# Performance work log

Measured on AMD Instinct MI355X. Metric: run time of the kernel, lower is better.

The kernel has to match this reference:

```python
import jax, jax.numpy as jnp
import numpy as np

B, IN, CTRL, M, V, OUT = 2048, 64, 512, 1024, 64, 64


def setup_inputs() -> dict:
    key = jax.random.key(0)
    ks = jax.random.split(key, 20)
    s = 0.05  # small param scale for numerical stability

    def rn(k, shape, scale):
        return jax.random.normal(k, shape, dtype=jnp.float32) * scale

    return {
        # forward args
        "x": rn(ks[0], (B, IN), 1.0),
        "h_prev": rn(ks[1], (B, CTRL), 0.1),
        "c_prev": rn(ks[2], (B, CTRL), 0.1),
        "read_weights_prev": jax.nn.softmax(rn(ks[3], (B, M), 1.0), axis=1),
        # parameters
        "memory": rn(ks[4], (M, V), 1.0),
        "W_ih": rn(ks[5], (4 * CTRL, IN + V), s),
        "b_ih": rn(ks[6], (4 * CTRL,), s),
        "W_hh": rn(ks[7], (4 * CTRL, CTRL), s),
        "b_hh": rn(ks[8], (4 * CTRL,), s),
        "W_read": rn(ks[9], (M, CTRL), s),
        "b_read": rn(ks[10], (M,), s),
        "W_write": rn(ks[11], (M, CTRL), s),
        "b_write": rn(ks[12], (M,), s),
        "W_erase": rn(ks[13], (V, CTRL), s),
        "b_erase": rn(ks[14], (V,), s),
        "W_add": rn(ks[15], (V, CTRL), s),
        "b_add": rn(ks[16], (V,), s),
        "W_out": rn(ks[17], (OUT, CTRL + V), s),
        "b_out": rn(ks[18], (OUT,), s),
    }


def reference(x, h_prev, c_prev, read_weights_prev, memory,
              W_ih, b_ih, W_hh, b_hh,
              W_read, b_read, W_write, b_write,
              W_erase, b_erase, W_add, b_add,
              W_out, b_out):
    # read with previous weights on pre-write memory: [B,M] @ [M,V] -> [B,V]
    read_prev = read_weights_prev @ memory
    inp = jnp.concatenate([x, read_prev], axis=1)  # [B, IN+V]

    # LSTMCell (PyTorch gate order: i, f, g, o)
    gates = inp @ W_ih.T + b_ih + h_prev @ W_hh.T + b_hh  # [B, 4*CTRL]
    i, f, g, o = jnp.split(gates, 4, axis=1)
    i = jax.nn.sigmoid(i)
    f = jax.nn.sigmoid(f)
    g = jnp.tanh(g)
    o = jax.nn.sigmoid(o)
    c = f * c_prev + i * g
    h = o * jnp.tanh(c)

    # addressing + erase/add vectors
    read_w = jax.nn.softmax(h @ W_read.T + b_read, axis=1)    # [B,M]
    write_w = jax.nn.softmax(h @ W_write.T + b_write, axis=1)  # [B,M]
    erase = jax.nn.sigmoid(h @ W_erase.T + b_erase)            # [B,V]
    add = jnp.tanh(h @ W_add.T + b_add)                        # [B,V]

    # outer-product erase/add memory update: [B,M,V]
    w = write_w[:, :, None]
    mem_new = memory[None, :, :] * (1.0 - w * erase[:, None, :]) + w * add[:, None, :]

    # read with new weights on post-write memory
    read_new = jnp.einsum('bm,bmv->bv', read_w, mem_new)

    out = jnp.concatenate([h, read_new], axis=1) @ W_out.T + b_out  # [B,OUT]
    return out
```

## Files before the change

### kernel.cpp

```cpp
#include <hip/hip_runtime.h>
#include <hip/hip_bf16.h>


typedef unsigned short u16;
typedef __attribute__((ext_vector_type(8))) short bf16x8;
typedef __attribute__((ext_vector_type(4))) float f32x4;

#define MFMA_BF16(a, b, c) __builtin_amdgcn_mfma_f32_16x16x32_bf16((a), (b), (c), 0, 0, 0)
#define LDW 136

__device__ __forceinline__ u16 f2bf(float f) {
    union { float f; unsigned int u; } a; a.f = f;
    return (u16)((a.u + 0x7FFFu + ((a.u >> 16) & 1u)) >> 16);
}

__device__ __forceinline__ void pack_store4(float a0, float a1, float a2, float a3, u16* d) {
    union { __hip_bfloat162 h[2]; uint2 u; } cv;
    cv.h[0] = __float22bfloat162_rn(make_float2(a0, a1));
    cv.h[1] = __float22bfloat162_rn(make_float2(a2, a3));
    *(uint2*)d = cv.u;
}

__device__ __forceinline__ void cvt4(const float* __restrict__ s, u16* __restrict__ d) {
    float4 v = *(const float4*)s;
// ... 41 lines not shown

__device__ __forceinline__ float sigf(float x) { return 1.f / (1.f + __expf(-x)); }
__device__ __forceinline__ float fast_tanh(float x) { return 1.f - 2.f / (__expf(2.f * x) + 1.f); }

__device__ __forceinline__ float wave_max(float v) {
#pragma unroll
    for (int o = 32; o > 0; o >>= 1) v = fmaxf(v, __shfl_xor(v, o, 64));
    return v;
}
__device__ __forceinline__ float wave_sum(float v) {
#pragma unroll
    for (int o = 32; o > 0; o >>= 1) v += __shfl_xor(v, o, 64);
    return v;
}

__global__ __launch_bounds__(256) void k_pre(
    const float* __restrict__ x, const float* __restrict__ h_prev, const float* __restrict__ rwp,
    const float* __restrict__ memory, const float* __restrict__ W_ih, const float* __restrict__ W_hh,
    const float* __restrict__ W_read, const float* __restrict__ W_write, const float* __restrict__ W_erase,
    const float* __restrict__ W_add, const float* __restrict__ W_out,
    u16* inp_h, u16* wcat, u16* Wcat2, u16* Wo_rn, u16* memt, float* rp)
{
    __shared__ u16 As[64 * LDW];
    __shared__ u16 Bs[64 * LDW];
    const int tid = threadIdx.x;

    if (blockIdx.x < 128) {
        const int mb = blockIdx.x & 31, ks = blockIdx.x >> 5;
        const int w = tid >> 6, lane = tid & 63;
        const int lrow = lane & 15, lq = lane >> 4;
        const int m0 = mb * 64, k0 = ks * 256;
        const int m_loc = tid >> 1, v0 = (tid & 1) * 32;
        f32x4 acc[4] = {};
        for (int kt = 0; kt < 2; ++kt) {
#pragma unroll
            for (int i = 0; i < 4; ++i) {
                int idx = i * 256 + tid, r = idx >> 4, c = (idx & 15) * 8;
                *(uint4*)(&As[r * LDW + c]) = cvt8u(rwp + (m0 + r) * 1024 + k0 + kt * 128 + c);
            }
#pragma unroll
            for (int j = 0; j < 8; ++j) {
                float4 q = *(const float4*)(memory + (k0 + kt * 128 + m_loc) * 64 + v0 + 4 * j);
                Bs[(v0 + 4 * j + 0) * LDW + m_loc] = f2bf(q.x);
                Bs[(v0 + 4 * j + 1) * LDW + m_loc] = f2bf(q.y);
                Bs[(v0 + 4 * j + 2) * LDW + m_loc] = f2bf(q.z);
                Bs[(v0 + 4 * j + 3) * LDW + m_loc] = f2bf(q.w);
            }
            __syncthreads();
#pragma unroll
            for (int kk = 0; kk < 128; kk += 32) {
                bf16x8 a  = *(const bf16x8*)(&As[(16 * w + lrow) * LDW + kk + 8 * lq]);
                bf16x8 b0 = *(const bf16x8*)(&Bs[(lrow) * LDW + kk + 8 * lq]);
                bf16x8 b1 = *(const bf16x8*)(&Bs[(16 + lrow) * LDW + kk + 8 * lq]);
                bf16x8 b2 = *(const bf16x8*)(&Bs[(32 + lrow) * LDW + kk + 8 * lq]);
                bf16x8 b3 = *(const bf16x8*)(&Bs[(48 + lrow) * LDW + kk + 8 * lq]);
                acc[0] = MFMA_BF16(a, b0, acc[0]);
                acc[1] = MFMA_BF16(a, b1, acc[1]);
                acc[2] = MFMA_BF16(a, b2, acc[2]);
                acc[3] = MFMA_BF16(a, b3, acc[3]);
            }
            __syncthreads();
        }
        float* rps = rp + ks * 131072;
#pragma unroll
        for (int nj = 0; nj < 4; ++nj)
#pragma unroll
            for (int r = 0; r < 4; ++r) {
                int row = m0 + 16 * w + 4 * lq + r, col = 16 * nj + lrow;
                rps[row * 64 + col] = acc[nj][r];
            }
        return;
    }

    int t = (blockIdx.x - 128) * 256 + tid;
    if (t < 32768) { int r = t >> 4, c = (t & 15) * 4; cvt4(x + r * 64 + c, inp_h + r * 576 + c); return; }
    t -= 32768;
    if (t < 262144) { int r = t >> 7, c = (t & 127) * 4; cvt4(h_prev + r * 512 + c, inp_h + r * 576 + 64 + c); return; }
    t -= 262144;
    if (t < 65536) {
        int r = t >> 5, c = (t & 31) * 4;
        int g = r >> 9, j = r & 511;
        int rn = (j >> 4) * 64 + (g << 4) + (j & 15);
        int cd = (c < 64) ? c + 64 : c - 64;
        cvt4(W_ih + r * 128 + c, wcat + rn * 640 + cd); return;
    }
    t -= 65536;
    if (t < 262144) {
        int r = t >> 7, c = (t & 127) * 4;
        int g = r >> 9, j = r & 511;
        int rn = (j >> 4) * 64 + (g << 4) + (j & 15);
        cvt4(W_hh + r * 512 + c, wcat + rn * 640 + 128 + c); return;
    }
    t -= 262144;
    if (t < 131072) { cvt4(W_read + t * 4, Wcat2 + t * 4); return; }
    t -= 131072;
    if (t < 131072) { cvt4(W_write + t * 4, Wcat2 + 524288 + t * 4); return; }
    t -= 131072;
    if (t < 8192) { cvt4(W_erase + t * 4, Wcat2 + 1048576 + t * 4); return; }
    t -= 8192;
    if (t < 8192) { cvt4(W_add + t * 4, Wcat2 + 1081344 + t * 4); return; }
    t -= 8192;
    if (t < 9216) {
        int r = t / 144, c = (t % 144) * 4;
        if (c < 512) cvt4(W_out + r * 576 + c, Wcat2 + (2176 + r) * 512 + c);
        else         cvt4(W_out + r * 576 + c, Wo_rn + r * 64 + (c - 512));
        return;
    }
    t -= 9216;
    if (t < 16384) {
        int v = t >> 8, m = (t & 255) * 4;
        pack_store4(memory[m * 64 + v], memory[(m + 1) * 64 + v],
                    memory[(m + 2) * 64 + v], memory[(m + 3) * 64 + v], memt + v * 1024 + m);
    }
}

__global__ __launch_bounds__(256) void k_gates(const u16* __restrict__ inp_h, const float* __restrict__ rp,
                                               const u16* __restrict__ wcat,
                                               const float* __restrict__ b_ih, const float* __restrict__ b_hh,
                                               const float* __restrict__ c_prev, u16* __restrict__ hrn)
{
    __shared__ u16 As[128 * LDW];
    __shared__ u16 Bs[64 * LDW];
    const int tid = threadIdx.x, w = tid >> 6, lane = tid & 63;
    const int lrow = lane & 15, lq = lane >> 4;
    const int m0 = blockIdx.x * 128, bn = blockIdx.y;
    const u16* Bbase = wcat + bn * 64 * 640;
    f32x4 acc[2][4] = {};
    for (int kt = 0; kt < 5; ++kt) {
#pragma unroll
        for (int i = 0; i < 8; ++i) {
            int idx = i * 256 + tid, r = idx >> 4, c = (idx & 15) * 8;
            int ak = kt * 128 + c;
            uint4 v;
            if (ak < 64) v = cvt8u_sum4(rp, (m0 + r) * 64 + ak);
            else         v = *(const uint4*)(inp_h + (m0 + r) * 576 + (ak - 64));
            *(uint4*)(&As[r * LDW + c]) = v;
        }
#pragma unroll
        for (int i = 0; i < 4; ++i) {
            int idx = i * 256 + tid, r = idx >> 4, c = (idx & 15) * 8;
            *(uint4*)(&Bs[r * LDW + c]) = *(const uint4*)(Bbase + r * 640 + kt * 128 + c);
        }
        __syncthreads();
#pragma unroll
        for (int kk = 0; kk < 128; kk += 32) {
            bf16x8 a0 = *(const bf16x8*)(&As[(32 * w + lrow) * LDW + kk + 8 * lq]);
            bf16x8 a1 = *(const bf16x8*)(&As[(32 * w + 16 + lrow) * LDW + kk + 8 * lq]);
            bf16x8 b0 = *(const bf16x8*)(&Bs[(lrow) * LDW + kk + 8 * lq]);
            bf16x8 b1 = *(const bf16x8*)(&Bs[(16 + lrow) * LDW + kk + 8 * lq]);
            bf16x8 b2 = *(const bf16x8*)(&Bs[(32 + lrow) * LDW + kk + 8 * lq]);
            bf16x8 b3 = *(const bf16x8*)(&Bs[(48 + lrow) * LDW + kk + 8 * lq]);
            acc[0][0] = MFMA_BF16(a0, b0, acc[0][0]);
            acc[0][1] = MFMA_BF16(a0, b1, acc[0][1]);
            acc[0][2] = MFMA_BF16(a0, b2, acc[0][2]);
            acc[0][3] = MFMA_BF16(a0, b3, acc[0][3]);
            acc[1][0] = MFMA_BF16(a1, b0, acc[1][0]);
            acc[1][1] = MFMA_BF16(a1, b1, acc[1][1]);
            acc[1][2] = MFMA_BF16(a1, b2, acc[1][2]);
            acc[1][3] = MFMA_BF16(a1, b3, acc[1][3]);
        }
        __syncthreads();
    }
    const int j = bn * 16 + lrow;
    const float bI = b_ih[j] + b_hh[j];
    const float bF = b_ih[512 + j] + b_hh[512 + j];
    const float bG = b_ih[1024 + j] + b_hh[1024 + j];
    const float bO = b_ih[1536 + j] + b_hh[1536 + j];
#pragma unroll
    for (int mi = 0; mi < 2; ++mi)
#pragma unroll
        for (int r = 0; r < 4; ++r) {
            int row = m0 + 32 * w + 16 * mi + 4 * lq + r;
            float ig = sigf(acc[mi][0][r] + bI);
            float fg = sigf(acc[mi][1][r] + bF);
            float gg = fast_tanh(acc[mi][2][r] + bG);
            float og = sigf(acc[mi][3][r] + bO);
            float c = fg * c_prev[row * 512 + j] + ig * gg;
            hrn[row * 512 + j] = f2bf(og * fast_tanh(c));
        }
}

__global__ __launch_bounds__(256) void k_heads(const u16* __restrict__ hrn, const u16* __restrict__ Wcat2,
                                               const float* __restrict__ b_read, const float* __restrict__ b_write,
                                               const float* __restrict__ b_erase, const float* __restrict__ b_add,
                                               const float* __restrict__ b_out,
                                               u16* __restrict__ pre_r, u16* __restrict__ pre_w,
                                               float* __restrict__ erase, float* __restrict__ add,
                                               float* __restrict__ out)
{
    __shared__ u16 As[128 * LDW];
    __shared__ u16 Bs[64 * LDW];
    const int tid = threadIdx.x, w = tid >> 6, lane = tid & 63;
    const int lrow = lane & 15, lq = lane >> 4;
    const int m0 = blockIdx.x * 128, bn = blockIdx.y;
    const u16* Bbase = Wcat2 + bn * 64 * 512;
    f32x4 acc[2][4] = {};
    for (int kt = 0; kt < 4; ++kt) {
#pragma unroll
        for (int i = 0; i < 8; ++i) {
            int idx = i * 256 + tid, r = idx >> 4, c = (idx & 15) * 8;
            *(uint4*)(&As[r * LDW + c]) = *(const uint4*)(hrn + (m0 + r) * 512 + kt * 128 + c);
        }
#pragma unroll
        for (int i = 0; i < 4; ++i) {
            int idx = i * 256 + tid, r = idx >> 4, c = (idx & 15) * 8;
            *(uint4*)(&Bs[r * LDW + c]) = *(const uint4*)(Bbase + r * 512 + kt * 128 + c);
        }
        __syncthreads();
#pragma unroll
        for (int kk = 0; kk < 128; kk += 32) {
            bf16x8 a0 = *(const bf16x8*)(&As[(32 * w + lrow) * LDW + kk + 8 * lq]);
            bf16x8 a1 = *(const bf16x8*)(&As[(32 * w + 16 + lrow) * LDW + kk + 8 * lq]);
            bf16x8 b0 = *(const bf16x8*)(&Bs[(lrow) * LDW + kk + 8 * lq]);
            bf16x8 b1 = *(const bf16x8*)(&Bs[(16 + lrow) * LDW + kk + 8 * lq]);
            bf16x8 b2 = *(const bf16x8*)(&Bs[(32 + lrow) * LDW + kk + 8 * lq]);
            bf16x8 b3 = *(const bf16x8*)(&Bs[(48 + lrow) * LDW + kk + 8 * lq]);
            acc[0][0] = MFMA_BF16(a0, b0, acc[0][0]);
            acc[0][1] = MFMA_BF16(a0, b1, acc[0][1]);
            acc[0][2] = MFMA_BF16(a0, b2, acc[0][2]);
            acc[0][3] = MFMA_BF16(a0, b3, acc[0][3]);
            acc[1][0] = MFMA_BF16(a1, b0, acc[1][0]);
            acc[1][1] = MFMA_BF16(a1, b1, acc[1][1]);
            acc[1][2] = MFMA_BF16(a1, b2, acc[1][2]);
            acc[1][3] = MFMA_BF16(a1, b3, acc[1][3]);
        }
        __syncthreads();
    }
#pragma unroll
    for (int mi = 0; mi < 2; ++mi)
#pragma unroll
        for (int nj = 0; nj < 4; ++nj)
#pragma unroll
            for (int r = 0; r < 4; ++r) {
                int row = m0 + 32 * w + 16 * mi + 4 * lq + r;
                int col = bn * 64 + 16 * nj + lrow;
                float v = acc[mi][nj][r];
                if (bn < 16)       pre_r[row * 1024 + col] = f2bf(v + b_read[col]);
                else if (bn < 32)  pre_w[row * 1024 + (col - 1024)] = f2bf(v + b_write[col - 1024]);
                else if (bn == 32) erase[row * 64 + (col - 2048)] = sigf(v + b_erase[col - 2048]);
                else if (bn == 33) add[row * 64 + (col - 2112)] = fast_tanh(v + b_add[col - 2112]);
                else               out[row * 64 + (col - 2176)] = v + b_out[col - 2176];
            }
}

__global__ __launch_bounds__(256) void k_softmax(const u16* __restrict__ pr, const u16* __restrict__ pw,
                                                 u16* __restrict__ rw_bf, u16* __restrict__ rw2_bf,
                                                 float* __restrict__ s)
{
    int b = blockIdx.x, tid = threadIdx.x, w = tid >> 6, lane = tid & 63;
    float4 vr = bf4_to_f4(*(const uint2*)(pr + b * 1024 + tid * 4));
    float4 vw = bf4_to_f4(*(const uint2*)(pw + b * 1024 + tid * 4));
    float mr = fmaxf(fmaxf(vr.x, vr.y), fmaxf(vr.z, vr.w));
    float mw = fmaxf(fmaxf(vw.x, vw.y), fmaxf(vw.z, vw.w));
    mr = wave_max(mr); mw = wave_max(mw);
    __shared__ float red[4][4];
    if (lane == 0) { red[0][w] = mr; red[1][w] = mw; }
    __syncthreads();
    mr = fmaxf(fmaxf(red[0][0], red[0][1]), fmaxf(red[0][2], red[0][3]));
    mw = fmaxf(fmaxf(red[1][0], red[1][1]), fmaxf(red[1][2], red[1][3]));
    float er[4] = {__expf(vr.x - mr), __expf(vr.y - mr), __expf(vr.z - mr), __expf(vr.w - mr)};
    float ew[4] = {__expf(vw.x - mw), __expf(vw.y - mw), __expf(vw.z - mw), __expf(vw.w - mw)};
    float sr = er[0] + er[1] + er[2] + er[3];
    float sw = ew[0] + ew[1] + ew[2] + ew[3];
    sr = wave_sum(sr); sw = wave_sum(sw);
    __syncthreads();
    if (lane == 0) { red[2][w] = sr; red[3][w] = sw; }
    __syncthreads();
    sr = red[2][0] + red[2][1] + red[2][2] + red[2][3];
    sw = red[3][0] + red[3][1] + red[3][2] + red[3][3];
    float isr = 1.f / sr, isw = 1.f / sw, ss = 0.f;
    float a[4], r2[4];
#pragma unroll
    for (int i = 0; i < 4; ++i) {
        a[i] = er[i] * isr;
        r2[i] = a[i] * (ew[i] * isw);
        ss += r2[i];
    }
    pack_store4(a[0], a[1], a[2], a[3], rw_bf + b * 1024 + tid * 4);
    pack_store4(r2[0], r2[1], r2[2], r2[3], rw2_bf + b * 1024 + tid * 4);
    ss = wave_sum(ss);
    __syncthreads();
    if (lane == 0) red[0][w] = ss;
    __syncthreads();
    if (tid == 0) s[b] = red[0][0] + red[0][1] + red[0][2] + red[0][3];
}

__global__ __launch_bounds__(256) void k_rnout(const u16* __restrict__ rw, const u16* __restrict__ rw2,
                                               const u16* __restrict__ memt, const u16* __restrict__ Wo_rn,
                                               const float* __restrict__ erase, const float* __restrict__ add,
                                               const float* __restrict__ s, float* __restrict__ out)
{
    __shared__ u16 As1[32 * LDW];
    __shared__ u16 As2[32 * LDW];
    __shared__ u16 Bs[64 * LDW];
    __shared__ u16 Ps[32 * 72];
    const int tid = threadIdx.x, w = tid >> 6, lane = tid & 63;
    const int lrow = lane & 15, lq = lane >> 4;
    const int m0 = blockIdx.x * 32, k0 = blockIdx.y * 256;
    const int mt = w & 1, nb = (w >> 1) * 2;

    f32x4 a1[2] = {}, a2[2] = {};
    for (int kt = 0; kt < 2; ++kt) {
#pragma unroll
        for (int i = 0; i < 2; ++i) {
            int idx = i * 256 + tid, r = idx >> 4, c = (idx & 15) * 8;
            *(uint4*)(&As1[r * LDW + c]) = *(const uint4*)(rw + (m0 + r) * 1024 + k0 + kt * 128 + c);
            *(uint4*)(&As2[r * LDW + c]) = *(const uint4*)(rw2 + (m0 + r) * 1024 + k0 + kt * 128 + c);
        }
#pragma unroll
        for (int i = 0; i < 4; ++i) {
            int idx = i * 256 + tid, r = idx >> 4, c = (idx & 15) * 8;
            *(uint4*)(&Bs[r * LDW + c]) = *(const uint4*)(memt + r * 1024 + k0 + kt * 128 + c);
        }
        __syncthreads();
#pragma unroll
        for (int kk = 0; kk < 128; kk += 32) {
            bf16x8 a  = *(const bf16x8*)(&As1[(16 * mt + lrow) * LDW + kk + 8 * lq]);
            bf16x8 c2 = *(const bf16x8*)(&As2[(16 * mt + lrow) * LDW + kk + 8 * lq]);
            bf16x8 b0 = *(const bf16x8*)(&Bs[(16 * nb + lrow) * LDW + kk + 8 * lq]);
            bf16x8 b1 = *(const bf16x8*)(&Bs[(16 * (nb + 1) + lrow) * LDW + kk + 8 * lq]);
            a1[0] = MFMA_BF16(a, b0, a1[0]);
            a1[1] = MFMA_BF16(a, b1, a1[1]);
            a2[0] = MFMA_BF16(c2, b0, a2[0]);
            a2[1] = MFMA_BF16(c2, b1, a2[1]);
        }
        __syncthreads();
    }
#pragma unroll
    for (int i = 0; i < 2; ++i) {
        int idx = i * 256 + tid, r = idx >> 3, c = (idx & 7) * 8;
        *(uint4*)(&Bs[r * LDW + c]) = *(const uint4*)(Wo_rn + r * 64 + c);
    }
#pragma unroll
    for (int j = 0; j < 2; ++j)
#pragma unroll
        for (int r = 0; r < 4; ++r) {
            int row_l = 16 * mt + 4 * lq + r, col = 16 * (nb + j) + lrow;
            int row_g = m0 + row_l;
            float p = a1[j][r] - erase[row_g * 64 + col] * a2[j][r];
            if (blockIdx.y == 0) p += add[row_g * 64 + col] * s[row_g];
            Ps[row_l * 72 + col] = f2bf(p);
        }
    __syncthreads();
    f32x4 o[2] = {};
#pragma unroll
    for (int kk = 0; kk < 64; kk += 32) {
        bf16x8 a  = *(const bf16x8*)(&Ps[(16 * mt + lrow) * 72 + kk + 8 * lq]);
        bf16x8 b0 = *(const bf16x8*)(&Bs[(16 * nb + lrow) * LDW + kk + 8 * lq]);
        bf16x8 b1 = *(const bf16x8*)(&Bs[(16 * (nb + 1) + lrow) * LDW + kk + 8 * lq]);
        o[0] = MFMA_BF16(a, b0, o[0]);
        o[1] = MFMA_BF16(a, b1, o[1]);
    }
#pragma unroll
    for (int j = 0; j < 2; ++j)
#pragma unroll
        for (int r = 0; r < 4; ++r) {
            int row_g = m0 + 16 * mt + 4 * lq + r, col = 16 * (nb + j) + lrow;
            atomicAdd(&out[row_g * 64 + col], o[j][r]);
        }
}

extern "C" void kernel_launch(void* const* d_in, const int* in_sizes, int n_in,
                              void* d_out, int out_size, void* d_ws, size_t ws_size,
                              hipStream_t stream)
{
    const float* x        = (const float*)d_in[0];
    const float* h_prev   = (const float*)d_in[1];
    const float* c_prev   = (const float*)d_in[2];
    const float* rwp      = (const float*)d_in[3];
    const float* memory   = (const float*)d_in[4];
    const float* W_ih     = (const float*)d_in[5];
    const float* b_ih     = (const float*)d_in[6];
    const float* W_hh     = (const float*)d_in[7];
    const float* b_hh     = (const float*)d_in[8];
    const float* W_read   = (const float*)d_in[9];
    const float* b_read   = (const float*)d_in[10];
    const float* W_write  = (const float*)d_in[11];
    const float* b_write  = (const float*)d_in[12];
    const float* W_erase  = (const float*)d_in[13];
    const float* b_erase  = (const float*)d_in[14];
    const float* W_add    = (const float*)d_in[15];
    const float* b_add    = (const float*)d_in[16];
    const float* W_out    = (const float*)d_in[17];
    const float* b_out    = (const float*)d_in[18];
    float* out = (float*)d_out;

    char* wsp = (char*)d_ws;
    u16*   inp_h  = (u16*)(wsp + 0);
    u16*   wcat   = (u16*)(wsp + 2359296);
    u16*   memt   = (u16*)(wsp + 4980736);
    u16*   Wcat2  = (u16*)(wsp + 5111808);
    u16*   Wo_rn  = (u16*)(wsp + 7405568);
    float* rp     = (float*)(wsp + 7413760);
    u16*   hrn    = (u16*)(wsp + 9510912);
    u16*   pre_r  = (u16*)(wsp + 11608064);
    u16*   pre_w  = (u16*)(wsp + 15802368);
    float* erase  = (float*)(wsp + 19996672);
    float* add    = (float*)(wsp + 20520960);
    u16*   rw_bf  = (u16*)(wsp + 21045248);
    u16*   rw2_bf = (u16*)(wsp + 25239552);
    float* s_buf  = (float*)(wsp + 29433856);

    k_pre<<<3748, 256, 0, stream>>>(x, h_prev, rwp, memory, W_ih, W_hh, W_read, W_write,
                                    W_erase, W_add, W_out,
                                    inp_h, wcat, Wcat2, Wo_rn, memt, rp);
    k_gates<<<dim3(16, 32), 256, 0, stream>>>(inp_h, rp, wcat, b_ih, b_hh, c_prev, hrn);
    k_heads<<<dim3(16, 35), 256, 0, stream>>>(hrn, Wcat2, b_read, b_write, b_erase, b_add, b_out,
                                              pre_r, pre_w, erase, add, out);
    k_softmax<<<2048, 256, 0, stream>>>(pre_r, pre_w, rw_bf, rw2_bf, s_buf);
    k_rnout<<<dim3(64, 4), 256, 0, stream>>>(rw_bf, rw2_bf, memt, Wo_rn, erase, add, s_buf, out);
}
```

Baseline: 159.8 us.

## Fuse five kernels into one persistent kernel with global atomic barriers

```diff
diff --git a/kernel.cpp b/kernel.cpp
--- a/kernel.cpp
+++ b/kernel.cpp
@@ -79,399 +79,408 @@
     return v;
 }
 
-__global__ __launch_bounds__(256) void k_pre(
-    const float* __restrict__ x, const float* __restrict__ h_prev, const float* __restrict__ rwp,
-    const float* __restrict__ memory, const float* __restrict__ W_ih, const float* __restrict__ W_hh,
-    const float* __restrict__ W_read, const float* __restrict__ W_write, const float* __restrict__ W_erase,
-    const float* __restrict__ W_add, const float* __restrict__ W_out,
-    u16* inp_h, u16* wcat, u16* Wcat2, u16* Wo_rn, u16* memt, float* rp)
+__device__ __forceinline__ void gbar(unsigned* cnt, int phase) {
+    __syncthreads();
+    if (threadIdx.x == 0) {
+        __hip_atomic_fetch_add(&cnt[phase], 1u, __ATOMIC_RELEASE, __HIP_MEMORY_SCOPE_AGENT);
+        while (__hip_atomic_load(&cnt[phase], __ATOMIC_ACQUIRE, __HIP_MEMORY_SCOPE_AGENT) < 256u)
+            __builtin_amdgcn_s_sleep(2);
+    }
+    __syncthreads();
+}
+
+struct KArgs {
+    const float *x, *h_prev, *c_prev, *rwp, *memory;
+    const float *W_ih, *b_ih, *W_hh, *b_hh;
+    const float *W_read, *b_read, *W_write, *b_write;
+    const float *W_erase, *b_erase, *W_add, *b_add, *W_out, *b_out;
+    float* out;
+    u16 *inp_h, *wcat, *Wcat2, *Wo_rn, *memt;
+    float* rp;
+    u16* hrn;
+    u16 *pre_r, *pre_w;
+    float *erase, *add;
+    u16 *rw_bf, *rw2_bf;
+    float* s_buf;
+    unsigned* bar;
+};
+
+__global__ void __launch_bounds__(256, 1) k_fused(KArgs A)
 {
-    __shared__ u16 As[64 * LDW];
-    __shared__ u16 Bs[64 * LDW];
+    __shared__ __align__(16) char smem[52224];
     const int tid = threadIdx.x;
-
-    if (blockIdx.x < 128) {
-        const int mb = blockIdx.x & 31, ks = blockIdx.x >> 5;
-        const int w = tid >> 6, lane = tid & 63;
-        const int lrow = lane & 15, lq = lane >> 4;
-        const int m0 = mb * 64, k0 = ks * 256;
-        const int m_loc = tid >> 1, v0 = (tid & 1) * 32;
-        f32x4 acc[4] = {};
+    const int w = tid >> 6, lane = tid & 63;
+    const int lrow = lane & 15, lq = lane >> 4;
+    const int bid = blockIdx.x;
+
+    {
+        u16* As = (u16*)smem;
+        u16* Bs = (u16*)(smem + 17408);
+        for (int vb = bid; vb < 3748; vb += 256) {
+            if (vb < 128) {
+                const int mb = vb & 31, ks = vb >> 5;
+                const int m0 = mb * 64, k0 = ks * 256;
+                const int m_loc = tid >> 1, v0 = (tid & 1) * 32;
+                f32x4 acc[4] = {};
+                for (int kt = 0; kt < 2; ++kt) {
+#pragma unroll
+                    for (int i = 0; i < 4; ++i) {
+                        int idx = i * 256 + tid, r = idx >> 4, c = (idx & 15) * 8;
+                        *(uint4*)(&As[r * LDW + c]) = cvt8u(A.rwp + (m0 + r) * 1024 + k0 + kt * 128 + c);
+                    }
+#pragma unroll
+                    for (int j = 0; j < 8; ++j) {
+                        float4 q = *(const float4*)(A.memory + (k0 + kt * 128 + m_loc) * 64 + v0 + 4 * j);
+                        Bs[(v0 + 4 * j + 0) * LDW + m_loc] = f2bf(q.x);
+                        Bs[(v0 + 4 * j + 1) * LDW + m_loc] = f2bf(q.y);
+                        Bs[(v0 + 4 * j + 2) * LDW + m_loc] = f2bf(q.z);
+                        Bs[(v0 + 4 * j + 3) * LDW + m_loc] = f2bf(q.w);
+                    }
+                    __syncthreads();
+#pragma unroll
+                    for (int kk = 0; kk < 128; kk += 32) {
+                        bf16x8 a  = *(const bf16x8*)(&As[(16 * w + lrow) * LDW + kk + 8 * lq]);
+                        bf16x8 b0 = *(const bf16x8*)(&Bs[(lrow) * LDW + kk + 8 * lq]);
+                        bf16x8 b1 = *(const bf16x8*)(&Bs[(16 + lrow) * LDW + kk + 8 * lq]);
+                        bf16x8 b2 = *(const bf16x8*)(&Bs[(32 + lrow) * LDW + kk + 8 * lq]);
+                        bf16x8 b3 = *(const bf16x8*)(&Bs[(48 + lrow) * LDW + kk + 8 * lq]);
+                        acc[0] = MFMA_BF16(a, b0, acc[0]);
+                        acc[1] = MFMA_BF16(a, b1, acc[1]);
+                        acc[2] = MFMA_BF16(a, b2, acc[2]);
+                        acc[3] = MFMA_BF16(a, b3, acc[3]);
+                    }
+                    __syncthreads();
+                }
+                float* rps = A.rp + ks * 131072;
+#pragma unroll
+                for (int nj = 0; nj < 4; ++nj)
+#pragma unroll
+                    for (int r = 0; r < 4; ++r) {
+                        int row = m0 + 16 * w + 4 * lq + r, col = 16 * nj + lrow;
+                        rps[row * 64 + col] = acc[nj][r];
+                    }
+                continue;
+            }
+            int t = (vb - 128) * 256 + tid;
+            if (t < 32768) { int r = t >> 4, c = (t & 15) * 4; cvt4(A.x + r * 64 + c, A.inp_h + r * 576 + c); continue; }
+            t -= 32768;
+            if (t < 262144) { int r = t >> 7, c = (t & 127) * 4; cvt4(A.h_prev + r * 512 + c, A.inp_h + r * 576 + 64 + c); continue; }
+            t -= 262144;
+            if (t < 65536) {
+                int r = t >> 5, c = (t & 31) * 4;
+                int g = r >> 9, j = r & 511;
+                int rn = (j >> 4) * 64 + (g << 4) + (j & 15);
+                int cd = (c < 64) ? c + 64 : c - 64;
+                cvt4(A.W_ih + r * 128 + c, A.wcat + rn * 640 + cd); continue;
+            }
+            t -= 65536;
+            if (t < 262144) {
+                int r = t >> 7, c = (t & 127) * 4;
+                int g = r >> 9, j = r & 511;
+                int rn = (j >> 4) * 64 + (g << 4) + (j & 15);
+                cvt4(A.W_hh + r * 512 + c, A.wcat + rn * 640 + 128 + c); continue;
+            }
+            t -= 262144;
+            if (t < 131072) { cvt4(A.W_read + t * 4, A.Wcat2 + t * 4); continue; }
+            t -= 131072;
+            if (t < 131072) { cvt4(A.W_write + t * 4, A.Wcat2 + 524288 + t * 4); continue; }
+            t -= 131072;
+            if (t < 8192) { cvt4(A.W_erase + t * 4, A.Wcat2 + 1048576 + t * 4); continue; }
+            t -= 8192;
+            if (t < 8192) { cvt4(A.W_add + t * 4, A.Wcat2 + 1081344 + t * 4); continue; }
+            t -= 8192;
+            if (t < 9216) {
+                int r = t / 144, c = (t % 144) * 4;
+                if (c < 512) cvt4(A.W_out + r * 576 + c, A.Wcat2 + (2176 + r) * 512 + c);
+                else         cvt4(A.W_out + r * 576 + c, A.Wo_rn + r * 64 + (c - 512));
+                continue;
+            }
+            t -= 9216;
+            if (t < 16384) {
+                int v = t >> 8, m = (t & 255) * 4;
+                pack_store4(A.memory[m * 64 + v], A.memory[(m + 1) * 64 + v],
+                            A.memory[(m + 2) * 64 + v], A.memory[(m + 3) * 64 + v], A.memt + v * 1024 + m);
+            }
+        }
+    }
+    gbar(A.bar, 0);
+
+    {
+        u16* As = (u16*)smem;
+        u16* Bs = (u16*)(smem + 34816);
+        for (int vb = bid; vb < 512; vb += 256) {
+            const int m0 = (vb & 15) * 128, bn = vb >> 4;
+            const u16* Bbase = A.wcat + bn * 64 * 640;
+            f32x4 acc[2][4] = {};
+            for (int kt = 0; kt < 5; ++kt) {
+#pragma unroll
+                for (int i = 0; i < 8; ++i) {
+                    int idx = i * 256 + tid, r = idx >> 4, c = (idx & 15) * 8;
+                    int ak = kt * 128 + c;
+                    uint4 v;
+                    if (ak < 64) v = cvt8u_sum4(A.rp, (m0 + r) * 64 + ak);
+                    else         v = *(const uint4*)(A.inp_h + (m0 + r) * 576 + (ak - 64));
+                    *(uint4*)(&As[r * LDW + c]) = v;
+                }
+#pragma unroll
+                for (int i = 0; i < 4; ++i) {
+                    int idx = i * 256 + tid, r = idx >> 4, c = (idx & 15) * 8;
+                    *(uint4*)(&Bs[r * LDW + c]) = *(const uint4*)(Bbase + r * 640 + kt * 128 + c);
+                }
+                __syncthreads();
+#pragma unroll
+                for (int kk = 0; kk < 128; kk += 32) {
+                    bf16x8 a0 = *(const bf16x8*)(&As[(32 * w + lrow) * LDW + kk + 8 * lq]);
+                    bf16x8 a1 = *(const bf16x8*)(&As[(32 * w + 16 + lrow) * LDW + kk + 8 * lq]);
+                    bf16x8 b0 = *(const bf16x8*)(&Bs[(lrow) * LDW + kk + 8 * lq]);
+                    bf16x8 b1 = *(const bf16x8*)(&Bs[(16 + lrow) * LDW + kk + 8 * lq]);
+                    bf16x8 b2 = *(const bf16x8*)(&Bs[(32 + lrow) * LDW + kk + 8 * lq]);
+                    bf16x8 b3 = *(const bf16x8*)(&Bs[(48 + lrow) * LDW + kk + 8 * lq]);
+                    acc[0][0] = MFMA_BF16(a0, b0, acc[0][0]);
+                    acc[0][1] = MFMA_BF16(a0, b1, acc[0][1]);
+                    acc[0][2] = MFMA_BF16(a0, b2, acc[0][2]);
+                    acc[0][3] = MFMA_BF16(a0, b3, acc[0][3]);
+                    acc[1][0] = MFMA_BF16(a1, b0, acc[1][0]);
+                    acc[1][1] = MFMA_BF16(a1, b1, acc[1][1]);
+                    acc[1][2] = MFMA_BF16(a1, b2, acc[1][2]);
+                    acc[1][3] = MFMA_BF16(a1, b3, acc[1][3]);
+                }
+                __syncthreads();
+            }
+            const int j = bn * 16 + lrow;
+            const float bI = A.b_ih[j] + A.b_hh[j];
+            const float bF = A.b_ih[512 + j] + A.b_hh[512 + j];
+            const float bG = A.b_ih[1024 + j] + A.b_hh[1024 + j];
+            const float bO = A.b_ih[1536 + j] + A.b_hh[1536 + j];
+#pragma unroll
+            for (int mi = 0; mi < 2; ++mi)
+#pragma unroll
+                for (int r = 0; r < 4; ++r) {
+                    int row = m0 + 32 * w + 16 * mi + 4 * lq + r;
+                    float ig = sigf(acc[mi][0][r] + bI);
+                    float fg = sigf(acc[mi][1][r] + bF);
+                    float gg = fast_tanh(acc[mi][2][r] + bG);
+                    float og = sigf(acc[mi][3][r] + bO);
+                    float c = fg * A.c_prev[row * 512 + j] + ig * gg;
+                    A.hrn[row * 512 + j] = f2bf(og * fast_tanh(c));
+                }
+        }
+    }
+    gbar(A.bar, 1);
+
+    {
+        u16* As = (u16*)smem;
+        u16* Bs = (u16*)(smem + 34816);
+        for (int vb = bid; vb < 560; vb += 256) {
+            const int m0 = (vb & 15) * 128, bn = vb >> 4;
+            const u16* Bbase = A.Wcat2 + bn * 64 * 512;
+            f32x4 acc[2][4] = {};
+            for (int kt = 0; kt < 4; ++kt) {
+#pragma unroll
+                for (int i = 0; i < 8; ++i) {
+                    int idx = i * 256 + tid, r = idx >> 4, c = (idx & 15) * 8;
+                    *(uint4*)(&As[r * LDW + c]) = *(const uint4*)(A.hrn + (m0 + r) * 512 + kt * 128 + c);
+                }
+#pragma unroll
+                for (int i = 0; i < 4; ++i) {
+                    int idx = i * 256 + tid, r = idx >> 4, c = (idx & 15) * 8;
+                    *(uint4*)(&Bs[r * LDW + c]) = *(const uint4*)(Bbase + r * 512 + kt * 128 + c);
+                }
+                __syncthreads();
+#pragma unroll
+                for (int kk = 0; kk < 128; kk += 32) {
+                    bf16x8 a0 = *(const bf16x8*)(&As[(32 * w + lrow) * LDW + kk + 8 * lq]);
+                    bf16x8 a1 = *(const bf16x8*)(&As[(32 * w + 16 + lrow) * LDW + kk + 8 * lq]);
+                    bf16x8 b0 = *(const bf16x8*)(&Bs[(lrow) * LDW + kk + 8 * lq]);
+                    bf16x8 b1 = *(const bf16x8*)(&Bs[(16 + lrow) * LDW + kk + 8 * lq]);
+                    bf16x8 b2 = *(const bf16x8*)(&Bs[(32 + lrow) * LDW + kk + 8 * lq]);
+                    bf16x8 b3 = *(const bf16x8*)(&Bs[(48 + lrow) * LDW + kk + 8 * lq]);
+                    acc[0][0] = MFMA_BF16(a0, b0, acc[0][0]);
+                    acc[0][1] = MFMA_BF16(a0, b1, acc[0][1]);
+                    acc[0][2] = MFMA_BF16(a0, b2, acc[0][2]);
+                    acc[0][3] = MFMA_BF16(a0, b3, acc[0][3]);
+                    acc[1][0] = MFMA_BF16(a1, b0, acc[1][0]);
+                    acc[1][1] = MFMA_BF16(a1, b1, acc[1][1]);
+                    acc[1][2] = MFMA_BF16(a1, b2, acc[1][2]);
+                    acc[1][3] = MFMA_BF16(a1, b3, acc[1][3]);
+                }
+                __syncthreads();
+            }
+#pragma unroll
+            for (int mi = 0; mi < 2; ++mi)
+#pragma unroll
+                for (int nj = 0; nj < 4; ++nj)
+#pragma unroll
+                    for (int r = 0; r < 4; ++r) {
+                        int row = m0 + 32 * w + 16 * mi + 4 * lq + r;
+                        int col = bn * 64 + 16 * nj + lrow;
+                        float v = acc[mi][nj][r];
+                        if (bn < 16)       A.pre_r[row * 1024 + col] = f2bf(v + A.b_read[col]);
+                        else if (bn < 32)  A.pre_w[row * 1024 + (col - 1024)] = f2bf(v + A.b_write[col - 1024]);
+                        else if (bn == 32) A.erase[row * 64 + (col - 2048)] = sigf(v + A.b_erase[col - 2048]);
+                        else if (bn == 33) A.add[row * 64 + (col - 2112)] = fast_tanh(v + A.b_add[col - 2112]);
+                        else               A.out[row * 64 + (col - 2176)] = v + A.b_out[col - 2176];
+                    }
+        }
+    }
+    gbar(A.bar, 2);
+
+    {
+        float (*red)[4] = (float(*)[4])smem;
+        for (int b = bid; b < 2048; b += 256) {
+            float4 vr = bf4_to_f4(*(const uint2*)(A.pre_r + b * 1024 + tid * 4));
+            float4 vw = bf4_to_f4(*(const uint2*)(A.pre_w + b * 1024 + tid * 4));
+            float mr = fmaxf(fmaxf(vr.x, vr.y), fmaxf(vr.z, vr.w));
+            float mw = fmaxf(fmaxf(vw.x, vw.y), fmaxf(vw.z, vw.w));
+            mr = wave_max(mr); mw = wave_max(mw);
+            if (lane == 0) { red[0][w] = mr; red[1][w] = mw; }
+            __syncthreads();
+            mr = fmaxf(fmaxf(red[0][0], red[0][1]), fmaxf(red[0][2], red[0][3]));
+            mw = fmaxf(fmaxf(red[1][0], red[1][1]), fmaxf(red[1][2], red[1][3]));
+            float er[4] = {__expf(vr.x - mr), __expf(vr.y - mr), __expf(vr.z - mr), __expf(vr.w - mr)};
+            float ew[4] = {__expf(vw.x - mw), __expf(vw.y - mw), __expf(vw.z - mw), __expf(vw.w - mw)};
+            float sr = er[0] + er[1] + er[2] + er[3];
+            float sw = ew[0] + ew[1] + ew[2] + ew[3];
+            sr = wave_sum(sr); sw = wave_sum(sw);
+            __syncthreads();
+            if (lane == 0) { red[2][w] = sr; red[3][w] = sw; }
+            __syncthreads();
+            sr = red[2][0] + red[2][1] + red[2][2] + red[2][3];
+            sw = red[3][0] + red[3][1] + red[3][2] + red[3][3];
+            float isr = 1.f / sr, isw = 1.f / sw, ss = 0.f;
+            float a[4], r2[4];
+#pragma unroll
+            for (int i = 0; i < 4; ++i) {
+                a[i] = er[i] * isr;
+                r2[i] = a[i] * (ew[i] * isw);
+                ss += r2[i];
+            }
+            pack_store4(a[0], a[1], a[2], a[3], A.rw_bf + b * 1024 + tid * 4);
+            pack_store4(r2[0], r2[1], r2[2], r2[3], A.rw2_bf + b * 1024 + tid * 4);
+            ss = wave_sum(ss);
+            __syncthreads();
+            if (lane == 0) red[0][w] = ss;
+            __syncthreads();
+            if (tid == 0) A.s_buf[b] = red[0][0] + red[0][1] + red[0][2] + red[0][3];
+            __syncthreads();
+        }
+    }
+    gbar(A.bar, 3);
+
+    {
+        u16* As1 = (u16*)smem;
+        u16* As2 = (u16*)(smem + 8704);
+        u16* Bs  = (u16*)(smem + 17408);
+        u16* Ps  = (u16*)(smem + 34816);
+        const int m0 = (bid & 63) * 32, ks = bid >> 6;
+        const int k0 = ks * 256;
+        const int mt = w & 1, nb = (w >> 1) * 2;
+
+        f32x4 a1[2] = {}, a2[2] = {};
         for (int kt = 0; kt < 2; ++kt) {
+#pragma unroll
+            for (int i = 0; i < 2; ++i) {
+                int idx = i * 256 + tid, r = idx >> 4, c = (idx & 15) * 8;
+                *(uint4*)(&As1[r * LDW + c]) = *(const uint4*)(A.rw_bf + (m0 + r) * 1024 + k0 + kt * 128 + c);
+                *(uint4*)(&As2[r * LDW + c]) = *(const uint4*)(A.rw2_bf + (m0 + r) * 1024 + k0 + kt * 128 + c);
+            }
 #pragma unroll
             for (int i = 0; i < 4; ++i) {
                 int idx = i * 256 + tid, r = idx >> 4, c = (idx & 15) * 8;
-                *(uint4*)(&As[r * LDW + c]) = cvt8u(rwp + (m0 + r) * 1024 + k0 + kt * 128 + c);
-            }
-#pragma unroll
-            for (int j = 0; j < 8; ++j) {
-                float4 q = *(const float4*)(memory + (k0 + kt * 128 + m_loc) * 64 + v0 + 4 * j);
-                Bs[(v0 + 4 * j + 0) * LDW + m_loc] = f2bf(q.x);
-                Bs[(v0 + 4 * j + 1) * LDW + m_loc] = f2bf(q.y);
-                Bs[(v0 + 4 * j + 2) * LDW + m_loc] = f2bf(q.z);
-                Bs[(v0 + 4 * j + 3) * LDW + m_loc] = f2bf(q.w);
+                *(uint4*)(&Bs[r * LDW + c]) = *(const uint4*)(A.memt + r * 1024 + k0 + kt * 128 + c);
             }
             __syncthreads();
 #pragma unroll
             for (int kk = 0; kk < 128; kk += 32) {
-                bf16x8 a  = *(const bf16x8*)(&As[(16 * w + lrow) * LDW + kk + 8 * lq]);
-                bf16x8 b0 = *(const bf16x8*)(&Bs[(lrow) * LDW + kk + 8 * lq]);
-                bf16x8 b1 = *(const bf16x8*)(&Bs[(16 + lrow) * LDW + kk + 8 * lq]);
-                bf16x8 b2 = *(const bf16x8*)(&Bs[(32 + lrow) * LDW + kk + 8 * lq]);
-                bf16x8 b3 = *(const bf16x8*)(&Bs[(48 + lrow) * LDW + kk + 8 * lq]);
-                acc[0] = MFMA_BF16(a, b0, acc[0]);
-                acc[1] = MFMA_BF16(a, b1, acc[1]);
-                acc[2] = MFMA_BF16(a, b2, acc[2]);
-                acc[3] = MFMA_BF16(a, b3, acc[3]);
-            }
-            __syncthreads();
-        }
-        float* rps = rp + ks * 131072;
-#pragma unroll
-        for (int nj = 0; nj < 4; ++nj)
+                bf16x8 a  = *(const bf16x8*)(&As1[(16 * mt + lrow) * LDW + kk + 8 * lq]);
+                bf16x8 c2 = *(const bf16x8*)(&As2[(16 * mt + lrow) * LDW + kk + 8 * lq]);
+                bf16x8 b0 = *(const bf16x8*)(&Bs[(16 * nb + lrow) * LDW + kk + 8 * lq]);
+                bf16x8 b1 = *(const bf16x8*)(&Bs[(16 * (nb + 1) + lrow) * LDW + kk + 8 * lq]);
+                a1[0] = MFMA_BF16(a, b0, a1[0]);
+                a1[1] = MFMA_BF16(a, b1, a1[1]);
+                a2[0] = MFMA_BF16(c2, b0, a2[0]);
+                a2[1] = MFMA_BF16(c2, b1, a2[1]);
+            }
+            __syncthreads();
+        }
+#pragma unroll
+        for (int i = 0; i < 2; ++i) {
+            int idx = i * 256 + tid, r = idx >> 3, c = (idx & 7) * 8;
+            *(uint4*)(&Bs[r * LDW + c]) = *(const uint4*)(A.Wo_rn + r * 64 + c);
+        }
+#pragma unroll
+        for (int j = 0; j < 2; ++j)
 #pragma unroll
             for (int r = 0; r < 4; ++r) {
-                int row = m0 + 16 * w + 4 * lq + r, col = 16 * nj + lrow;
-                rps[row * 64 + col] = acc[nj][r];
-            }
-        return;
-    }
-
-    int t = (blockIdx.x - 128) * 256 + tid;
-    if (t < 32768) { int r = t >> 4, c = (t & 15) * 4; cvt4(x + r * 64 + c, inp_h + r * 576 + c); return; }
-    t -= 32768;
-    if (t < 262144) { int r = t >> 7, c = (t & 127) * 4; cvt4(h_prev + r * 512 + c, inp_h + r * 576 + 64 + c); return; }
-    t -= 262144;
-    if (t < 65536) {
-        int r = t >> 5, c = (t & 31) * 4;
-        int g = r >> 9, j = r & 511;
-        int rn = (j >> 4) * 64 + (g << 4) + (j & 15);
-        int cd = (c < 64) ? c + 64 : c - 64;
-        cvt4(W_ih + r * 128 + c, wcat + rn * 640 + cd); return;
-    }
-    t -= 65536;
-    if (t < 262144) {
-        int r = t >> 7, c = (t & 127) * 4;
-        int g = r >> 9, j = r & 511;
-        int rn = (j >> 4) * 64 + (g << 4) + (j & 15);
-        cvt4(W_hh + r * 512 + c, wcat + rn * 640 + 128 + c); return;
-    }
-    t -= 262144;
-    if (t < 131072) { cvt4(W_read + t * 4, Wcat2 + t * 4); return; }
-    t -= 131072;
-    if (t < 131072) { cvt4(W_write + t * 4, Wcat2 + 524288 + t * 4); return; }
-    t -= 131072;
-    if (t < 8192) { cvt4(W_erase + t * 4, Wcat2 + 1048576 + t * 4); return; }
-    t -= 8192;
-    if (t < 8192) { cvt4(W_add + t * 4, Wcat2 + 1081344 + t * 4); return; }
-    t -= 8192;
-    if (t < 9216) {
-        int r = t / 144, c = (t % 144) * 4;
-        if (c < 512) cvt4(W_out + r * 576 + c, Wcat2 + (2176 + r) * 512 + c);
-        else         cvt4(W_out + r * 576 + c, Wo_rn + r * 64 + (c - 512));
-        return;
-    }
-    t -= 9216;
-    if (t < 16384) {
-        int v = t >> 8, m = (t & 255) * 4;
-        pack_store4(memory[m * 64 + v], memory[(m + 1) * 64 + v],
-                    memory[(m + 2) * 64 + v], memory[(m + 3) * 64 + v], memt + v * 1024 + m);
-    }
-}
-
-__global__ __launch_bounds__(256) void k_gates(const u16* __restrict__ inp_h, const float* __restrict__ rp,
-                                               const u16* __restrict__ wcat,
-                                               const float* __restrict__ b_ih, const float* __restrict__ b_hh,
-                                               const float* __restrict__ c_prev, u16* __restrict__ hrn)
-{
-    __shared__ u16 As[128 * LDW];
-    __shared__ u16 Bs[64 * LDW];
-    const int tid = threadIdx.x, w = tid >> 6, lane = tid & 63;
-    const int lrow = lane & 15, lq = lane >> 4;
-    const int m0 = blockIdx.x * 128, bn = blockIdx.y;
-    const u16* Bbase = wcat + bn * 64 * 640;
-    f32x4 acc[2][4] = {};
-    for (int kt = 0; kt < 5; ++kt) {
-#pragma unroll
-        for (int i = 0; i < 8; ++i) {
-            int idx = i * 256 + tid, r = idx >> 4, c = (idx & 15) * 8;
-            int ak = kt * 128 + c;
-            uint4 v;
-            if (ak < 64) v = cvt8u_sum4(rp, (m0 + r) * 64 + ak);
-            else         v = *(const uint4*)(inp_h + (m0 + r) * 576 + (ak - 64));
-            *(uint4*)(&As[r * LDW + c]) = v;
-        }
-#pragma unroll
-        for (int i = 0; i < 4; ++i) {
-            int idx = i * 256 + tid, r = idx >> 4, c = (idx & 15) * 8;
-            *(uint4*)(&Bs[r * LDW + c]) = *(const uint4*)(Bbase + r * 640 + kt * 128 + c);
-        }
+                int row_l = 16 * mt + 4 * lq + r, col = 16 * (nb + j) + lrow;
+                int row_g = m0 + row_l;
+                float p = a1[j][r] - A.erase[row_g * 64 + col] * a2[j][r];
+                if (ks == 0) p += A.add[row_g * 64 + col] * A.s_buf[row_g];
+                Ps[row_l * 72 + col] = f2bf(p);
+            }
         __syncthreads();
-#pragma unroll
-        for (int kk = 0; kk < 128; kk += 32) {
-            bf16x8 a0 = *(const bf16x8*)(&As[(32 * w + lrow) * LDW + kk + 8 * lq]);
-            bf16x8 a1 = *(const bf16x8*)(&As[(32 * w + 16 + lrow) * LDW + kk + 8 * lq]);
-            bf16x8 b0 = *(const bf16x8*)(&Bs[(lrow) * LDW + kk + 8 * lq]);
-            bf16x8 b1 = *(const bf16x8*)(&Bs[(16 + lrow) * LDW + kk + 8 * lq]);
-            bf16x8 b2 = *(const bf16x8*)(&Bs[(32 + lrow) * LDW + kk + 8 * lq]);
-            bf16x8 b3 = *(const bf16x8*)(&Bs[(48 + lrow) * LDW + kk + 8 * lq]);
-            acc[0][0] = MFMA_BF16(a0, b0, acc[0][0]);
-            acc[0][1] = MFMA_BF16(a0, b1, acc[0][1]);
-            acc[0][2] = MFMA_BF16(a0, b2, acc[0][2]);
-            acc[0][3] = MFMA_BF16(a0, b3, acc[0][3]);
-            acc[1][0] = MFMA_BF16(a1, b0, acc[1][0]);
-            acc[1][1] = MFMA_BF16(a1, b1, acc[1][1]);
-            acc[1][2] = MFMA_BF16(a1, b2, acc[1][2]);
-            acc[1][3] = MFMA_BF16(a1, b3, acc[1][3]);
-        }
-        __syncthreads();
-    }
-    const int j = bn * 16 + lrow;
-    const float bI = b_ih[j] + b_hh[j];
-    const float bF = b_ih[512 + j] + b_hh[512 + j];
-    const float bG = b_ih[1024 + j] + b_hh[1024 + j];
-    const float bO = b_ih[1536 + j] + b_hh[1536 + j];
-#pragma unroll
-    for (int mi = 0; mi < 2; ++mi)
-#pragma unroll
-        for (int r = 0; r < 4; ++r) {
-            int row = m0 + 32 * w + 16 * mi + 4 * lq + r;
-            float ig = sigf(acc[mi][0][r] + bI);
-            float fg = sigf(acc[mi][1][r] + bF);
-            float gg = fast_tanh(acc[mi][2][r] + bG);
-            float og = sigf(acc[mi][3][r] + bO);
-            float c = fg * c_prev[row * 512 + j] + ig * gg;
-            hrn[row * 512 + j] = f2bf(og * fast_tanh(c));
-        }
-}
-
-__global__ __launch_bounds__(256) void k_heads(const u16* __restrict__ hrn, const u16* __restrict__ Wcat2,
-                                               const float* __restrict__ b_read, const float* __restrict__ b_write,
-                                               const float* __restrict__ b_erase, const float* __restrict__ b_add,
-                                               const float* __restrict__ b_out,
-                                               u16* __restrict__ pre_r, u16* __restrict__ pre_w,
-                                               float* __restrict__ erase, float* __restrict__ add,
-                                               float* __restrict__ out)
-{
-    __shared__ u16 As[128 * LDW];
-    __shared__ u16 Bs[64 * LDW];
-    const int tid = threadIdx.x, w = tid >> 6, lane = tid & 63;
-    const int lrow = lane & 15, lq = lane >> 4;
-    const int m0 = blockIdx.x * 128, bn = blockIdx.y;
-    const u16* Bbase = Wcat2 + bn * 64 * 512;
-    f32x4 acc[2][4] = {};
-    for (int kt = 0; kt < 4; ++kt) {
-#pragma unroll
-        for (int i = 0; i < 8; ++i) {
-            int idx = i * 256 + tid, r = idx >> 4, c = (idx & 15) * 8;
-            *(uint4*)(&As[r * LDW + c]) = *(const uint4*)(hrn + (m0 + r) * 512 + kt * 128 + c);
-        }
-#pragma unroll
-        for (int i = 0; i < 4; ++i) {
-            int idx = i * 256 + tid, r = idx >> 4, c = (idx & 15) * 8;
-            *(uint4*)(&Bs[r * LDW + c]) = *(const uint4*)(Bbase + r * 512 + kt * 128 + c);
-        }
-        __syncthreads();
-#pragma unroll
-        for (int kk = 0; kk < 128; kk += 32) {
-            bf16x8 a0 = *(const bf16x8*)(&As[(32 * w + lrow) * LDW + kk + 8 * lq]);
-            bf16x8 a1 = *(const bf16x8*)(&As[(32 * w + 16 + lrow) * LDW + kk + 8 * lq]);
-            bf16x8 b0 = *(const bf16x8*)(&Bs[(lrow) * LDW + kk + 8 * lq]);
-            bf16x8 b1 = *(const bf16x8*)(&Bs[(16 + lrow) * LDW + kk + 8 * lq]);
-            bf16x8 b2 = *(const bf16x8*)(&Bs[(32 + lrow) * LDW + kk + 8 * lq]);
-            bf16x8 b3 = *(const bf16x8*)(&Bs[(48 + lrow) * LDW + kk + 8 * lq]);
-            acc[0][0] = MFMA_BF16(a0, b0, acc[0][0]);
-            acc[0][1] = MFMA_BF16(a0, b1, acc[0][1]);
-            acc[0][2] = MFMA_BF16(a0, b2, acc[0][2]);
-            acc[0][3] = MFMA_BF16(a0, b3, acc[0][3]);
-            acc[1][0] = MFMA_BF16(a1, b0, acc[1][0]);
-            acc[1][1] = MFMA_BF16(a1, b1, acc[1][1]);
-            acc[1][2] = MFMA_BF16(a1, b2, acc[1][2]);
-            acc[1][3] = MFMA_BF16(a1, b3, acc[1][3]);
-        }
-        __syncthreads();
-    }
-#pragma unroll
-    for (int mi = 0; mi < 2; ++mi)
-#pragma unroll
-        for (int nj = 0; nj < 4; ++nj)
-#pragma unroll
-            for (int r = 0; r < 4; ++r) {
-                int row = m0 + 32 * w + 16 * mi + 4 * lq + r;
-                int col = bn * 64 + 16 * nj + lrow;
-                float v = acc[mi][nj][r];
-                if (bn < 16)       pre_r[row * 1024 + col] = f2bf(v + b_read[col]);
-                else if (bn < 32)  pre_w[row * 1024 + (col - 1024)] = f2bf(v + b_write[col - 1024]);
-                else if (bn == 32) erase[row * 64 + (col - 2048)] = sigf(v + b_erase[col - 2048]);
-                else if (bn == 33) add[row * 64 + (col - 2112)] = fast_tanh(v + b_add[col - 2112]);
-                else               out[row * 64 + (col - 2176)] = v + b_out[col - 2176];
-            }
-}
-
-__global__ __launch_bounds__(256) void k_softmax(const u16* __restrict__ pr, const u16* __restrict__ pw,
-                                                 u16* __restrict__ rw_bf, u16* __restrict__ rw2_bf,
-                                                 float* __restrict__ s)
-{
-    int b = blockIdx.x, tid = threadIdx.x, w = tid >> 6, lane = tid & 63;
-    float4 vr = bf4_to_f4(*(const uint2*)(pr + b * 1024 + tid * 4));
-    float4 vw = bf4_to_f4(*(const uint2*)(pw + b * 1024 + tid * 4));
-    float mr = fmaxf(fmaxf(vr.x, vr.y), fmaxf(vr.z, vr.w));
-    float mw = fmaxf(fmaxf(vw.x, vw.y), fmaxf(vw.z, vw.w));
-    mr = wave_max(mr); mw = wave_max(mw);
-    __shared__ float red[4][4];
-    if (lane == 0) { red[0][w] = mr; red[1][w] = mw; }
-    __syncthreads();
-    mr = fmaxf(fmaxf(red[0][0], red[0][1]), fmaxf(red[0][2], red[0][3]));
-    mw = fmaxf(fmaxf(red[1][0], red[1][1]), fmaxf(red[1][2], red[1][3]));
-    float er[4] = {__expf(vr.x - mr), __expf(vr.y - mr), __expf(vr.z - mr), __expf(vr.w - mr)};
-    float ew[4] = {__expf(vw.x - mw), __expf(vw.y - mw), __expf(vw.z - mw), __expf(vw.w - mw)};
-    float sr = er[0] + er[1] + er[2] + er[3];
-    float sw = ew[0] + ew[1] + ew[2] + ew[3];
-    sr = wave_sum(sr); sw = wave_sum(sw);
-    __syncthreads();
-    if (lane == 0) { red[2][w] = sr; red[3][w] = sw; }
-    __syncthreads();
-    sr = red[2][0] + red[2][1] + red[2][2] + red[2][3];
-    sw = red[3][0] + red[3][1] + red[3][2] + red[3][3];
-    float isr = 1.f / sr, isw = 1.f / sw, ss = 0.f;
-    float a[4], r2[4];
-#pragma unroll
-    for (int i = 0; i < 4; ++i) {
-        a[i] = er[i] * isr;
-        r2[i] = a[i] * (ew[i] * isw);
-        ss += r2[i];
-    }
-    pack_store4(a[0], a[1], a[2], a[3], rw_bf + b * 1024 + tid * 4);
-    pack_store4(r2[0], r2[1], r2[2], r2[3], rw2_bf + b * 1024 + tid * 4);
-    ss = wave_sum(ss);
-    __syncthreads();
-    if (lane == 0) red[0][w] = ss;
-    __syncthreads();
-    if (tid == 0) s[b] = red[0][0] + red[0][1] + red[0][2] + red[0][3];
-}
-
-__global__ __launch_bounds__(256) void k_rnout(const u16* __restrict__ rw, const u16* __restrict__ rw2,
-                                               const u16* __restrict__ memt, const u16* __restrict__ Wo_rn,
-                                               const float* __restrict__ erase, const float* __restrict__ add,
-                                               const float* __restrict__ s, float* __restrict__ out)
-{
-    __shared__ u16 As1[32 * LDW];
-    __shared__ u16 As2[32 * LDW];
-    __shared__ u16 Bs[64 * LDW];
-    __shared__ u16 Ps[32 * 72];
-    const int tid = threadIdx.x, w = tid >> 6, lane = tid & 63;
-    const int lrow = lane & 15, lq = lane >> 4;
-    const int m0 = blockIdx.x * 32, k0 = blockIdx.y * 256;
-    const int mt = w & 1, nb = (w >> 1) * 2;
-
-    f32x4 a1[2] = {}, a2[2] = {};
-    for (int kt = 0; kt < 2; ++kt) {
-#pragma unroll
-        for (int i = 0; i < 2; ++i) {
-            int idx = i * 256 + tid, r = idx >> 4, c = (idx & 15) * 8;
-            *(uint4*)(&As1[r * LDW + c]) = *(const uint4*)(rw + (m0 + r) * 1024 + k0 + kt * 128 + c);
-            *(uint4*)(&As2[r * LDW + c]) = *(const uint4*)(rw2 + (m0 + r) * 1024 + k0 + kt * 128 + c);
-        }
-#pragma unroll
-        for (int i = 0; i < 4; ++i) {
-            int idx = i * 256 + tid, r = idx >> 4, c = (idx & 15) * 8;
-            *(uint4*)(&Bs[r * LDW + c]) = *(const uint4*)(memt + r * 1024 + k0 + kt * 128 + c);
-        }
-        __syncthreads();
-#pragma unroll
-        for (int kk = 0; kk < 128; kk += 32) {
-            bf16x8 a  = *(const bf16x8*)(&As1[(16 * mt + lrow) * LDW + kk + 8 * lq]);
-            bf16x8 c2 = *(const bf16x8*)(&As2[(16 * mt + lrow) * LDW + kk + 8 * lq]);
+        f32x4 o[2] = {};
+#pragma unroll
+        for (int kk = 0; kk < 64; kk += 32) {
+            bf16x8 a  = *(const bf16x8*)(&Ps[(16 * mt + lrow) * 72 + kk + 8 * lq]);
             bf16x8 b0 = *(const bf16x8*)(&Bs[(16 * nb + lrow) * LDW + kk + 8 * lq]);
             bf16x8 b1 = *(const bf16x8*)(&Bs[(16 * (nb + 1) + lrow) * LDW + kk + 8 * lq]);
-            a1[0] = MFMA_BF16(a, b0, a1[0]);
-            a1[1] = MFMA_BF16(a, b1, a1[1]);
-            a2[0] = MFMA_BF16(c2, b0, a2[0]);
-            a2[1] = MFMA_BF16(c2, b1, a2[1]);
-        }
-        __syncthreads();
-    }
-#pragma unroll
-    for (int i = 0; i < 2; ++i) {
-        int idx = i * 256 + tid, r = idx >> 3, c = (idx & 7) * 8;
-        *(uint4*)(&Bs[r * LDW + c]) = *(const uint4*)(Wo_rn + r * 64 + c);
-    }
-#pragma unroll
-    for (int j = 0; j < 2; ++j)
-#pragma unroll
-        for (int r = 0; r < 4; ++r) {
-            int row_l = 16 * mt + 4 * lq + r, col = 16 * (nb + j) + lrow;
-            int row_g = m0 + row_l;
-            float p = a1[j][r] - erase[row_g * 64 + col] * a2[j][r];
-            if (blockIdx.y == 0) p += add[row_g * 64 + col] * s[row_g];
-            Ps[row_l * 72 + col] = f2bf(p);
-        }
-    __syncthreads();
-    f32x4 o[2] = {};
-#pragma unroll
-    for (int kk = 0; kk < 64; kk += 32) {
-        bf16x8 a  = *(const bf16x8*)(&Ps[(16 * mt + lrow) * 72 + kk + 8 * lq]);
-        bf16x8 b0 = *(const bf16x8*)(&Bs[(16 * nb + lrow) * LDW + kk + 8 * lq]);
-        bf16x8 b1 = *(const bf16x8*)(&Bs[(16 * (nb + 1) + lrow) * LDW + kk + 8 * lq]);
-        o[0] = MFMA_BF16(a, b0, o[0]);
-        o[1] = MFMA_BF16(a, b1, o[1]);
-    }
-#pragma unroll
-    for (int j = 0; j < 2; ++j)
-#pragma unroll
-        for (int r = 0; r < 4; ++r) {
-            int row_g = m0 + 16 * mt + 4 * lq + r, col = 16 * (nb + j) + lrow;
-            atomicAdd(&out[row_g * 64 + col], o[j][r]);
-        }
+            o[0] = MFMA_BF16(a, b0, o[0]);
+            o[1] = MFMA_BF16(a, b1, o[1]);
+        }
+#pragma unroll
+        for (int j = 0; j < 2; ++j)
+#pragma unroll
+            for (int r = 0; r < 4; ++r) {
+                int row_g = m0 + 16 * mt + 4 * lq + r, col = 16 * (nb + j) + lrow;
+                atomicAdd(&A.out[row_g * 64 + col], o[j][r]);
+            }
+    }
 }
 
 extern "C" void kernel_launch(void* const* d_in, const int* in_sizes, int n_in,
                               void* d_out, int out_size, void* d_ws, size_t ws_size,
                               hipStream_t stream)
 {
-    const float* x        = (const float*)d_in[0];
-    const float* h_prev   = (const float*)d_in[1];
-    const float* c_prev   = (const float*)d_in[2];
-    const float* rwp      = (const float*)d_in[3];
-    const float* memory   = (const float*)d_in[4];
-    const float* W_ih     = (const float*)d_in[5];
-    const float* b_ih     = (const float*)d_in[6];
-    const float* W_hh     = (const float*)d_in[7];
-    const float* b_hh     = (const float*)d_in[8];
-    const float* W_read   = (const float*)d_in[9];
-    const float* b_read   = (const float*)d_in[10];
-    const float* W_write  = (const float*)d_in[11];
-    const float* b_write  = (const float*)d_in[12];
-    const float* W_erase  = (const float*)d_in[13];
-    const float* b_erase  = (const float*)d_in[14];
-    const float* W_add    = (const float*)d_in[15];
-    const float* b_add    = (const float*)d_in[16];
-    const float* W_out    = (const float*)d_in[17];
-    const float* b_out    = (const float*)d_in[18];
-    float* out = (float*)d_out;
-
     char* wsp = (char*)d_ws;
-    u16*   inp_h  = (u16*)(wsp + 0);
-    u16*   wcat   = (u16*)(wsp + 2359296);
-    u16*   memt   = (u16*)(wsp + 4980736);
-    u16*   Wcat2  = (u16*)(wsp + 5111808);
-    u16*   Wo_rn  = (u16*)(wsp + 7405568);
-    float* rp     = (float*)(wsp + 7413760);
-    u16*   hrn    = (u16*)(wsp + 9510912);
-    u16*   pre_r  = (u16*)(wsp + 11608064);
-    u16*   pre_w  = (u16*)(wsp + 15802368);
-    float* erase  = (float*)(wsp + 19996672);
-    float* add    = (float*)(wsp + 20520960);
-    u16*   rw_bf  = (u16*)(wsp + 21045248);
-    u16*   rw2_bf = (u16*)(wsp + 25239552);
-    float* s_buf  = (float*)(wsp + 29433856);
-
-    k_pre<<<3748, 256, 0, stream>>>(x, h_prev, rwp, memory, W_ih, W_hh, W_read, W_write,
-                                    W_erase, W_add, W_out,
-                                    inp_h, wcat, Wcat2, Wo_rn, memt, rp);
-    k_gates<<<dim3(16, 32), 256, 0, stream>>>(inp_h, rp, wcat, b_ih, b_hh, c_prev, hrn);
-    k_heads<<<dim3(16, 35), 256, 0, stream>>>(hrn, Wcat2, b_read, b_write, b_erase, b_add, b_out,
-                                              pre_r, pre_w, erase, add, out);
-    k_softmax<<<2048, 256, 0, stream>>>(pre_r, pre_w, rw_bf, rw2_bf, s_buf);
-    k_rnout<<<dim3(64, 4), 256, 0, stream>>>(rw_bf, rw2_bf, memt, Wo_rn, erase, add, s_buf, out);
-}
+    KArgs ka;
+    ka.x       = (const float*)d_in[0];
+    ka.h_prev  = (const float*)d_in[1];
+    ka.c_prev  = (const float*)d_in[2];
+    ka.rwp     = (const float*)d_in[3];
+    ka.memory  = (const float*)d_in[4];
+    ka.W_ih    = (const float*)d_in[5];
+    ka.b_ih    = (const float*)d_in[6];
+    ka.W_hh    = (const float*)d_in[7];
+    ka.b_hh    = (const float*)d_in[8];
+    ka.W_read  = (const float*)d_in[9];
+    ka.b_read  = (const float*)d_in[10];
+    ka.W_write = (const float*)d_in[11];
+    ka.b_write = (const float*)d_in[12];
+    ka.W_erase = (const float*)d_in[13];
+    ka.b_erase = (const float*)d_in[14];
+    ka.W_add   = (const float*)d_in[15];
+    ka.b_add   = (const float*)d_in[16];
+    ka.W_out   = (const float*)d_in[17];
+    ka.b_out   = (const float*)d_in[18];
+    ka.out     = (float*)d_out;
+
+    ka.inp_h  = (u16*)(wsp + 0);
+    ka.wcat   = (u16*)(wsp + 2359296);
+    ka.memt   = (u16*)(wsp + 4980736);
+    ka.Wcat2  = (u16*)(wsp + 5111808);
+    ka.Wo_rn  = (u16*)(wsp + 7405568);
+    ka.rp     = (float*)(wsp + 7413760);
+    ka.hrn    = (u16*)(wsp + 9510912);
+    ka.pre_r  = (u16*)(wsp + 11608064);
+    ka.pre_w  = (u16*)(wsp + 15802368);
+    ka.erase  = (float*)(wsp + 19996672);
+    ka.add    = (float*)(wsp + 20520960);
+    ka.rw_bf  = (u16*)(wsp + 21045248);
+    ka.rw2_bf = (u16*)(wsp + 25239552);
+    ka.s_buf  = (float*)(wsp + 29433856);
+    ka.bar    = (unsigned*)(wsp + 29442048);
+
+    hipMemsetAsync(wsp + 29442048, 0, 16, stream);
+    k_fused<<<256, 256, 0, stream>>>(ka);
+}
```

Measured after the change: 321.0 us. 2.01x slower.
